# Kernel optimization log

Hardware: AMD Instinct MI355X
Metric: run time of the kernel (lower is better)

## Reference

```python
import jax, jax.numpy as jnp
import numpy as np

HEAD_SIZE = 64
N_EMBD = 1024
BLOCK_SIZE = 2048


def setup_inputs() -> dict:
    key = jax.random.key(0)
    kx, kk, kq, kv = jax.random.split(key, 4)
    B, T = 8, 2048
    x = jax.random.normal(kx, (B, T, N_EMBD), dtype=jnp.float32)
    # nnx.Linear kernels have shape (in_features, out_features); lecun-normal-ish scale
    s = 1.0 / np.sqrt(N_EMBD)
    Wk = jax.random.normal(kk, (N_EMBD, HEAD_SIZE), dtype=jnp.float32) * s
    Wq = jax.random.normal(kq, (N_EMBD, HEAD_SIZE), dtype=jnp.float32) * s
    Wv = jax.random.normal(kv, (N_EMBD, HEAD_SIZE), dtype=jnp.float32) * s
    return {"x": x, "Wk": Wk, "Wq": Wq, "Wv": Wv}


def reference(x, Wk, Wq, Wv):
    B, T, C = x.shape
    k = jnp.einsum("btc,ch->bth", x, Wk)  # [B,T,H]
    q = jnp.einsum("btc,ch->bth", x, Wq)
    v = jnp.einsum("btc,ch->bth", x, Wv)
    # NOTE: original scales by C**-0.5 where C = n_embd (not head_size)
    scale = jnp.float32(C) ** -0.5
    wei = jnp.einsum("bth,bsh->bts", q, k) * scale  # [B,T,T]
    causal = jnp.tril(jnp.ones((T, T), dtype=bool))
    wei = jnp.where(causal, wei, -jnp.inf)
    wei = jax.nn.softmax(wei, axis=-1)
    # dropout_rate = 0.0 -> identity
    out = jnp.einsum("bts,bsh->bth", wei, v)  # [B,T,H]
    return out
```

## Files before the change

### kernel.cpp

```cpp
#include <hip/hip_runtime.h>
#include <hip/hip_bf16.h>

#define TT 2048
#define BATCH 8
#define MROWS (BATCH*TT)
#define AW 8

typedef __attribute__((ext_vector_type(8))) short bf16x8;
typedef __attribute__((ext_vector_type(4))) short s16x4;
typedef __attribute__((ext_vector_type(4))) float f32x4;

__device__ __forceinline__ short f2bf(float f) {
    union { __hip_bfloat16 h; short s; } u;
    u.h = __float2bfloat16(f);
    return u.s;
}
__device__ __forceinline__ float bf2f(short s) {
    union { unsigned u; float f; } u;
    u.u = ((unsigned)(unsigned short)s) << 16;
    return u.f;
}

typedef __attribute__((address_space(3))) unsigned int       lds_u32_t;
typedef const __attribute__((address_space(1))) unsigned int g_u32_t;
__device__ __forceinline__ void gl_lds16(const void* g, void* l) {
    __builtin_amdgcn_global_load_lds((g_u32_t*)g, (lds_u32_t*)l, 16, 0, 0);
}

__global__ __launch_bounds__(256) void wtrans_kernel(
    const float* __restrict__ Wk, const float* __restrict__ Wq,
    const float* __restrict__ Wv, short* __restrict__ wt)
{
    __shared__ float tile[64][68];
    const int mat = blockIdx.x >> 4;
    const int k0  = (blockIdx.x & 15) * 64;
    const float* W = (mat == 0) ? Wq : (mat == 1) ? Wk : Wv;
    const float scl = (mat == 0) ? 0.04508422002778011f : 1.0f;
    const int t = threadIdx.x;
    const int row = t >> 2, quad = t & 3;
    #pragma unroll
    for (int i = 0; i < 4; i++) {
        float4 v = *(const float4*)(W + (size_t)(k0 + row) * 64 + quad * 16 + i * 4);
        *(float4*)&tile[row][quad * 16 + i * 4] = v;
    }
    __syncthreads();
    short tmp[16];
    #pragma unroll
    for (int j = 0; j < 16; j++) tmp[j] = f2bf(tile[quad * 16 + j][row] * scl);
    short* dst = wt + (size_t)(mat * 64 + row) * 1024 + k0 + quad * 16;
    #pragma unroll
    for (int j2 = 0; j2 < 2; j2++) {
        bf16x8 o;
        #pragma unroll
        for (int jj = 0; jj < 8; jj++) o[jj] = tmp[j2 * 8 + jj];
        *(bf16x8*)(dst + j2 * 8) = o;
    }
}

__global__ __launch_bounds__(256, 2) void proj_kernel(
    const float* __restrict__ x, const short* __restrict__ wt,
    short* __restrict__ qb, short* __restrict__ kb, short* __restrict__ vtb)
{
    __shared__ __align__(16) char lds[65536];

    const int tid  = threadIdx.x;
    const int lane = tid & 63, w = tid >> 6;
    const int l15  = lane & 15, g = lane >> 4;
    const int x7   = l15 & 7;
    const int wr   = w & 1;
    const int wc   = w >> 1;
    const int r0   = blockIdx.x * 32;

    const float* ag[2]; unsigned aOff[2];
    #pragma unroll
    for (int j = 0; j < 2; j++) {
        const int jp   = w * 2 + j;
        const int row  = jp * 4 + (lane >> 4);
        const int slot = (lane & 15) ^ (row & 7);
        ag[j]   = x + (size_t)(r0 + row) * 1024 + slot * 4;
        aOff[j] = jp * 1024;
    }
    const short* bg[6]; unsigned bOff[6];
    #pragma unroll
    for (int j = 0; j < 6; j++) {
        const int jp   = w * 6 + j;
        const int row  = jp * 8 + (lane >> 3);
        const int slot = (lane & 7) ^ (row & 7);
        bg[j]   = wt + (size_t)row * 1024 + slot * 8;
        bOff[j] = jp * 1024;
    }

    f32x4 acc[6];
    #pragma unroll
    for (int nt = 0; nt < 6; nt++) acc[nt] = (f32x4){0.f, 0.f, 0.f, 0.f};

    #pragma unroll
    for (int j = 0; j < 2; j++) gl_lds16(ag[j], lds + aOff[j]);
    #pragma unroll
    for (int j = 0; j < 6; j++) gl_lds16(bg[j], lds + 16384 + bOff[j]);
    __syncthreads();

    #pragma unroll
    for (int ks = 0; ks < 16; ks++) {
        const int cur = ks & 1;

        if (ks < 15) {
            const int nb = cur ^ 1;
            #pragma unroll
            for (int j = 0; j < 2; j++)
                gl_lds16(ag[j] + (ks + 1) * 64, lds + nb * 8192 + aOff[j]);
            #pragma unroll
            for (int j = 0; j < 6; j++)
                gl_lds16(bg[j] + (ks + 1) * 64, lds + 16384 + nb * 24576 + bOff[j]);
        }

        const float* Ab = (const float*)(lds + cur * 8192);
        const short* Bb = (const short*)(lds + 16384 + cur * 24576);

        bf16x8 af[2];
        #pragma unroll
        for (int kc = 0; kc < 2; kc++) {
            const int arow = wr * 16 + l15;
            f32x4 lo = *(const f32x4*)(Ab + arow * 64 + ((kc * 8 + 2 * g)     ^ x7) * 4);
            f32x4 hi = *(const f32x4*)(Ab + arow * 64 + ((kc * 8 + 2 * g + 1) ^ x7) * 4);
            af[kc] = (bf16x8){ f2bf(lo[0]), f2bf(lo[1]), f2bf(lo[2]), f2bf(lo[3]),
                               f2bf(hi[0]), f2bf(hi[1]), f2bf(hi[2]), f2bf(hi[3]) };
        }
        bf16x8 bfr[6][2];
        #pragma unroll
        for (int nt = 0; nt < 6; nt++)
            #pragma unroll
            for (int kc = 0; kc < 2; kc++)
                bfr[nt][kc] = *(const bf16x8*)(
                    Bb + (wc * 96 + nt * 16 + l15) * 64 + ((kc * 4 + g) ^ x7) * 8);

        #pragma unroll
        for (int kc = 0; kc < 2; kc++)
            #pragma unroll
            for (int nt = 0; nt < 6; nt++)
                acc[nt] = __builtin_amdgcn_mfma_f32_16x16x32_bf16(
                    af[kc], bfr[nt][kc], acc[nt], 0, 0, 0);

        __syncthreads();
    }

    const int bi  = r0 >> 11;
    const int sl0 = r0 & 2047;
    short* vsl = (short*)lds;
    #pragma unroll
    for (int nt = 0; nt < 6; nt++) {
        const int c = wc * 96 + nt * 16 + l15;
        #pragma unroll
        for (int r = 0; r < 4; r++) {
            const int row = r0 + wr * 16 + g * 4 + r;
            const short v = f2bf(acc[nt][r]);
            if (c < 64)        qb[(size_t)row * 64 + c] = v;
            else if (c < 128)  kb[(size_t)row * 64 + (c - 64)] = v;
            else               vsl[(wr * 16 + g * 4 + r) * 66 + (c - 128)] = v;
        }
    }
    __syncthreads();
    {
        const int col = tid >> 2, seg = tid & 3;
        short tmp[8];
        #pragma unroll
        for (int j = 0; j < 8; j++) tmp[j] = vsl[(seg * 8 + j) * 66 + col];
        bf16x8 o;
        #pragma unroll
        for (int jj = 0; jj < 8; jj++) o[jj] = tmp[jj];
        *(bf16x8*)(vtb + ((size_t)bi * 64 + col) * TT + sl0 + seg * 8) = o;
    }
}

__global__ __launch_bounds__(512, 2)
void attn_kernel(
    const short* __restrict__ qb, const short* __restrict__ kb,
    const short* __restrict__ vtb, float* __restrict__ out)
{
    __shared__ __align__(16) char smem[AW * 4608];
    __shared__ float ml[AW][64];

    const int tid  = threadIdx.x;
    const int w    = tid >> 6, lane = tid & 63;
    const int l15  = lane & 15, g = lane >> 4;
    const int b    = blockIdx.x & 7;
    const int qt   = 63 - (blockIdx.x >> 3);
    const int r0   = qt * 32;
    const int nkv  = (r0 >> 6) + 1;

    short* ps = (short*)(smem + w * 4608);

    const short* q  = qb  + (size_t)b * TT * 64;
    const short* k  = kb  + (size_t)b * TT * 64;
    const short* vt = vtb + (size_t)b * 64 * TT;

    bf16x8 qf[2][2];
    #pragma unroll
    for (int rt = 0; rt < 2; rt++)
        #pragma unroll
        for (int kc = 0; kc < 2; kc++)
            qf[rt][kc] = *(const bf16x8*)(q + (size_t)(r0 + rt * 16 + l15) * 64 + kc * 32 + g * 8);

    f32x4 o[2][4];
    float m_[2] = { -INFINITY, -INFINITY };
    float l_[2] = { 0.f, 0.f };
    #pragma unroll
    for (int rt = 0; rt < 2; rt++)
        #pragma unroll
        for (int ht = 0; ht < 4; ht++) o[rt][ht] = (f32x4){0.f, 0.f, 0.f, 0.f};

    bf16x8 kf[4][2];
    if (w < nkv) {
        #pragma unroll
        for (int nt = 0; nt < 4; nt++)
            #pragma unroll
            for (int kc = 0; kc < 2; kc++)
                kf[nt][kc] = *(const bf16x8*)(
                    k + (size_t)(w * 64 + nt * 16 + l15) * 64 + kc * 32 + g * 8);
    }

    for (int t = w; t < nkv; t += AW) {
        const int s0 = t * 64;
        const bool diag = (t == nkv - 1);
        const bool more = (t + AW < nkv);

        f32x4 s[2][4];
        #pragma unroll
        for (int rt = 0; rt < 2; rt++)
            #pragma unroll
            for (int nt = 0; nt < 4; nt++) s[rt][nt] = (f32x4){0.f, 0.f, 0.f, 0.f};
        #pragma unroll
        for (int kc = 0; kc < 2; kc++)
            #pragma unroll
            for (int rt = 0; rt < 2; rt++)
                #pragma unroll
                for (int nt = 0; nt < 4; nt++)
                    s[rt][nt] = __builtin_amdgcn_mfma_f32_16x16x32_bf16(
                        kf[nt][kc], qf[rt][kc], s[rt][nt], 0, 0, 0);

        bf16x8 vf[4][2];
        #pragma unroll
        for (int ht = 0; ht < 4; ht++)
            #pragma unroll
            for (int kc = 0; kc < 2; kc++)
                vf[ht][kc] = *(const bf16x8*)(
                    vt + (size_t)(ht * 16 + l15) * TT + s0 + kc * 32 + g * 8);
        bf16x8 kfn[4][2];
        if (more) {
            #pragma unroll
            for (int nt = 0; nt < 4; nt++)
                #pragma unroll
                for (int kc = 0; kc < 2; kc++)
                    kfn[nt][kc] = *(const bf16x8*)(
                        k + (size_t)(s0 + AW * 64 + nt * 16 + l15) * 64 + kc * 32 + g * 8);
        }

        if (diag) {
            #pragma unroll
            for (int rt = 0; rt < 2; rt++) {
                const int qg = r0 + rt * 16 + l15;
                #pragma unroll
                for (int nt = 0; nt < 4; nt++)
                    #pragma unroll
                    for (int r = 0; r < 4; r++)
                        if (s0 + nt * 16 + g * 4 + r > qg) s[rt][nt][r] = -INFINITY;
            }
        }

        #pragma unroll
        for (int rt = 0; rt < 2; rt++) {
            float a0 = fmaxf(fmaxf(s[rt][0][0], s[rt][0][1]), fmaxf(s[rt][0][2], s[rt][0][3]));
            float a1 = fmaxf(fmaxf(s[rt][1][0], s[rt][1][1]), fmaxf(s[rt][1][2], s[rt][1][3]));
            float a2 = fmaxf(fmaxf(s[rt][2][0], s[rt][2][1]), fmaxf(s[rt][2][2], s[rt][2][3]));
            float a3 = fmaxf(fmaxf(s[rt][3][0], s[rt][3][1]), fmaxf(s[rt][3][2], s[rt][3][3]));
            float tm = fmaxf(fmaxf(a0, a1), fmaxf(a2, a3));
            tm = fmaxf(tm, __shfl_xor(tm, 16));
            tm = fmaxf(tm, __shfl_xor(tm, 32));

            const float mn = fmaxf(m_[rt], tm);
            const float al = __builtin_amdgcn_exp2f(m_[rt] - mn);
            m_[rt] = mn;

            #pragma unroll
            for (int nt = 0; nt < 4; nt++)
                #pragma unroll
                for (int r = 0; r < 4; r++)
                    s[rt][nt][r] = __builtin_amdgcn_exp2f(s[rt][nt][r] - mn);

            float b0 = (s[rt][0][0] + s[rt][0][1]) + (s[rt][0][2] + s[rt][0][3]);
            float b1 = (s[rt][1][0] + s[rt][1][1]) + (s[rt][1][2] + s[rt][1][3]);
            float b2 = (s[rt][2][0] + s[rt][2][1]) + (s[rt][2][2] + s[rt][2][3]);
            float b3 = (s[rt][3][0] + s[rt][3][1]) + (s[rt][3][2] + s[rt][3][3]);
            float ts = (b0 + b1) + (b2 + b3);
            ts += __shfl_xor(ts, 16);
            ts += __shfl_xor(ts, 32);
            l_[rt] = l_[rt] * al + ts;

            float ab[4];
            #pragma unroll
            for (int r = 0; r < 4; r++) ab[r] = __shfl(al, g * 4 + r);
            #pragma unroll
            for (int ht = 0; ht < 4; ht++)
                #pragma unroll
                for (int r = 0; r < 4; r++)
                    o[rt][ht][r] *= ab[r];

            #pragma unroll
            for (int nt = 0; nt < 4; nt++) {
                s16x4 pk = { f2bf(s[rt][nt][0]), f2bf(s[rt][nt][1]),
                             f2bf(s[rt][nt][2]), f2bf(s[rt][nt][3]) };
                *(s16x4*)&ps[(rt * 16 + l15) * 72 + nt * 16 + g * 4] = pk;
            }
        }

        bf16x8 pf[2][2];
        #pragma unroll
        for (int rt = 0; rt < 2; rt++)
            #pragma unroll
            for (int kc = 0; kc < 2; kc++)
                pf[rt][kc] = *(const bf16x8*)&ps[(rt * 16 + l15) * 72 + kc * 32 + g * 8];
        #pragma unroll
        for (int kc = 0; kc < 2; kc++)
            #pragma unroll
            for (int rt = 0; rt < 2; rt++)
                #pragma unroll
                for (int ht = 0; ht < 4; ht++)
                    o[rt][ht] = __builtin_amdgcn_mfma_f32_16x16x32_bf16(
                        pf[rt][kc], vf[ht][kc], o[rt][ht], 0, 0, 0);

        if (more) {
            #pragma unroll
            for (int nt = 0; nt < 4; nt++)
                #pragma unroll
                for (int kc = 0; kc < 2; kc++)
                    kf[nt][kc] = kfn[nt][kc];
        }
    }

    if (g == 0) {
        #pragma unroll
        for (int rt = 0; rt < 2; rt++) {
            ml[w][rt * 16 + l15]      = m_[rt];
            ml[w][32 + rt * 16 + l15] = l_[rt];
        }
    }
    short* pO = ps;
    #pragma unroll
    for (int rt = 0; rt < 2; rt++)
        #pragma unroll
        for (int ht = 0; ht < 4; ht++)
            #pragma unroll
            for (int r = 0; r < 4; r++)
                pO[(rt * 16 + g * 4 + r) * 68 + ht * 16 + l15] = f2bf(o[rt][ht][r]);
    __syncthreads();

    {
        const int row = tid >> 4, seg = tid & 15;
        float gm = -INFINITY;
        #pragma unroll
        for (int w2 = 0; w2 < AW; w2++) gm = fmaxf(gm, ml[w2][row]);
        float accL = 0.f;
        float accO[4] = {0.f, 0.f, 0.f, 0.f};
        #pragma unroll
        for (int w2 = 0; w2 < AW; w2++) {
            const float sc = __builtin_amdgcn_exp2f(ml[w2][row] - gm);
            accL = fmaf(sc, ml[w2][32 + row], accL);
            const s16x4 ov = *(const s16x4*)((const short*)(smem + w2 * 4608) + row * 68 + seg * 4);
            #pragma unroll
            for (int j = 0; j < 4; j++)
                accO[j] = fmaf(sc, bf2f(ov[j]), accO[j]);
        }
        const float inv = 1.f / accL;
        float4 res = make_float4(accO[0] * inv, accO[1] * inv, accO[2] * inv, accO[3] * inv);
        *(float4*)(out + ((size_t)b * TT + r0 + row) * 64 + seg * 4) = res;
    }
}

extern "C" void kernel_launch(void* const* d_in, const int* in_sizes, int n_in,
                              void* d_out, int out_size, void* d_ws, size_t ws_size,
                              hipStream_t stream) {
    const float* x  = (const float*)d_in[0];
    const float* Wk = (const float*)d_in[1];
    const float* Wq = (const float*)d_in[2];
    const float* Wv = (const float*)d_in[3];
    float* outp = (float*)d_out;

    short* wt  = (short*)d_ws;
    short* qb  = wt + (size_t)192 * 1024;
    short* kb  = qb + (size_t)MROWS * 64;
    short* vtb = kb + (size_t)MROWS * 64;

    wtrans_kernel<<<48, 256, 0, stream>>>(Wk, Wq, Wv, wt);
    proj_kernel<<<MROWS / 32, 256, 0, stream>>>(x, wt, qb, kb, vtb);
    attn_kernel<<<BATCH * 64, 512, 0, stream>>>(qb, kb, vtb, outp);
}
```

Baseline: 47.21 us.

## Enlarge projection tile to 64 rows and stage x as bf16 in LDS

The QKV projection kernel now uses 64-row blocks with 512 threads and a K-step of 128. Each wave computes a 2x3 grid of MFMA tiles, so every weight fragment is reused across two row tiles. x is loaded into registers, converted to bf16 once, and written to LDS after the MFMAs, which overlaps the global load with compute and halves A-tile LDS traffic. The cost is 128KB of LDS, which limits occupancy to about one block per CU, plus more register pressure.

```diff
diff --git a/kernel.cpp b/kernel.cpp
--- a/kernel.cpp
+++ b/kernel.cpp
@@ -57,11 +57,11 @@
     }
 }
 
-__global__ __launch_bounds__(256, 2) void proj_kernel(
+__global__ __launch_bounds__(512, 2) void proj_kernel(
     const float* __restrict__ x, const short* __restrict__ wt,
     short* __restrict__ qb, short* __restrict__ kb, short* __restrict__ vtb)
 {
-    __shared__ __align__(16) char lds[65536];
+    __shared__ __align__(16) char lds[131072];
 
     const int tid  = threadIdx.x;
     const int lane = tid & 63, w = tid >> 6;
@@ -69,78 +69,99 @@
     const int x7   = l15 & 7;
     const int wr   = w & 1;
     const int wc   = w >> 1;
-    const int r0   = blockIdx.x * 32;
-
-    const float* ag[2]; unsigned aOff[2];
-    #pragma unroll
-    for (int j = 0; j < 2; j++) {
-        const int jp   = w * 2 + j;
+    const int r0   = blockIdx.x * 64;
+
+    const int arow_s = tid >> 3, aseg = tid & 7;
+    const float* xsrc = x + (size_t)(r0 + arow_s) * 1024 + aseg * 16;
+    const int ac0 = ((aseg * 2)     ^ (arow_s & 7)) * 16;
+    const int ac1 = ((aseg * 2 + 1) ^ (arow_s & 7)) * 16;
+    char* const arow_lds0 = lds + arow_s * 256;
+
+    const short* bg[6]; unsigned bOff[6];
+    #pragma unroll
+    for (int j = 0; j < 6; j++) {
+        const int jp   = w * 6 + j;
         const int row  = jp * 4 + (lane >> 4);
         const int slot = (lane & 15) ^ (row & 7);
-        ag[j]   = x + (size_t)(r0 + row) * 1024 + slot * 4;
-        aOff[j] = jp * 1024;
-    }
-    const short* bg[6]; unsigned bOff[6];
-    #pragma unroll
-    for (int j = 0; j < 6; j++) {
-        const int jp   = w * 6 + j;
-        const int row  = jp * 8 + (lane >> 3);
-        const int slot = (lane & 7) ^ (row & 7);
         bg[j]   = wt + (size_t)row * 1024 + slot * 8;
-        bOff[j] = jp * 1024;
-    }
-
-    f32x4 acc[6];
-    #pragma unroll
-    for (int nt = 0; nt < 6; nt++) acc[nt] = (f32x4){0.f, 0.f, 0.f, 0.f};
-
-    #pragma unroll
-    for (int j = 0; j < 2; j++) gl_lds16(ag[j], lds + aOff[j]);
-    #pragma unroll
-    for (int j = 0; j < 6; j++) gl_lds16(bg[j], lds + 16384 + bOff[j]);
+        bOff[j] = 32768 + jp * 1024;
+    }
+
+    f32x4 acc[2][3];
+    #pragma unroll
+    for (int rt = 0; rt < 2; rt++)
+        #pragma unroll
+        for (int nt = 0; nt < 3; nt++) acc[rt][nt] = (f32x4){0.f, 0.f, 0.f, 0.f};
+
+    {
+        float4 a0 = *(const float4*)(xsrc);
+        float4 a1 = *(const float4*)(xsrc + 4);
+        float4 a2 = *(const float4*)(xsrc + 8);
+        float4 a3 = *(const float4*)(xsrc + 12);
+        #pragma unroll
+        for (int j = 0; j < 6; j++) gl_lds16(bg[j], lds + bOff[j]);
+        bf16x8 c0 = { f2bf(a0.x), f2bf(a0.y), f2bf(a0.z), f2bf(a0.w),
+                      f2bf(a1.x), f2bf(a1.y), f2bf(a1.z), f2bf(a1.w) };
+        bf16x8 c1 = { f2bf(a2.x), f2bf(a2.y), f2bf(a2.z), f2bf(a2.w),
+                      f2bf(a3.x), f2bf(a3.y), f2bf(a3.z), f2bf(a3.w) };
+        *(bf16x8*)(arow_lds0 + ac0) = c0;
+        *(bf16x8*)(arow_lds0 + ac1) = c1;
+    }
     __syncthreads();
 
     #pragma unroll
-    for (int ks = 0; ks < 16; ks++) {
+    for (int ks = 0; ks < 8; ks++) {
         const int cur = ks & 1;
-
-        if (ks < 15) {
-            const int nb = cur ^ 1;
-            #pragma unroll
-            for (int j = 0; j < 2; j++)
-                gl_lds16(ag[j] + (ks + 1) * 64, lds + nb * 8192 + aOff[j]);
+        const int nb  = cur ^ 1;
+
+        float4 a0, a1, a2, a3;
+        if (ks < 7) {
+            a0 = *(const float4*)(xsrc + (ks + 1) * 128);
+            a1 = *(const float4*)(xsrc + (ks + 1) * 128 + 4);
+            a2 = *(const float4*)(xsrc + (ks + 1) * 128 + 8);
+            a3 = *(const float4*)(xsrc + (ks + 1) * 128 + 12);
             #pragma unroll
             for (int j = 0; j < 6; j++)
-                gl_lds16(bg[j] + (ks + 1) * 64, lds + 16384 + nb * 24576 + bOff[j]);
-        }
-
-        const float* Ab = (const float*)(lds + cur * 8192);
-        const short* Bb = (const short*)(lds + 16384 + cur * 24576);
-
-        bf16x8 af[2];
-        #pragma unroll
-        for (int kc = 0; kc < 2; kc++) {
-            const int arow = wr * 16 + l15;
-            f32x4 lo = *(const f32x4*)(Ab + arow * 64 + ((kc * 8 + 2 * g)     ^ x7) * 4);
-            f32x4 hi = *(const f32x4*)(Ab + arow * 64 + ((kc * 8 + 2 * g + 1) ^ x7) * 4);
-            af[kc] = (bf16x8){ f2bf(lo[0]), f2bf(lo[1]), f2bf(lo[2]), f2bf(lo[3]),
-                               f2bf(hi[0]), f2bf(hi[1]), f2bf(hi[2]), f2bf(hi[3]) };
-        }
-        bf16x8 bfr[6][2];
-        #pragma unroll
-        for (int nt = 0; nt < 6; nt++)
-            #pragma unroll
-            for (int kc = 0; kc < 2; kc++)
+                gl_lds16(bg[j] + (ks + 1) * 128, lds + nb * 49152 + bOff[j]);
+        }
+
+        const char*  Ab = lds + cur * 16384;
+        const short* Bb = (const short*)(lds + 32768 + cur * 49152);
+
+        bf16x8 af[2][4];
+        #pragma unroll
+        for (int rt = 0; rt < 2; rt++) {
+            const int arow = wr * 32 + rt * 16 + l15;
+            #pragma unroll
+            for (int kc = 0; kc < 4; kc++)
+                af[rt][kc] = *(const bf16x8*)(
+                    Ab + arow * 256 + (((kc * 4 + g) ^ x7) * 16));
+        }
+        bf16x8 bfr[3][4];
+        #pragma unroll
+        for (int nt = 0; nt < 3; nt++)
+            #pragma unroll
+            for (int kc = 0; kc < 4; kc++)
                 bfr[nt][kc] = *(const bf16x8*)(
-                    Bb + (wc * 96 + nt * 16 + l15) * 64 + ((kc * 4 + g) ^ x7) * 8);
-
-        #pragma unroll
-        for (int kc = 0; kc < 2; kc++)
-            #pragma unroll
-            for (int nt = 0; nt < 6; nt++)
-                acc[nt] = __builtin_amdgcn_mfma_f32_16x16x32_bf16(
-                    af[kc], bfr[nt][kc], acc[nt], 0, 0, 0);
-
+                    Bb + (wc * 48 + nt * 16 + l15) * 128 + (((kc * 4 + g) ^ x7) * 8));
+
+        #pragma unroll
+        for (int kc = 0; kc < 4; kc++)
+            #pragma unroll
+            for (int rt = 0; rt < 2; rt++)
+                #pragma unroll
+                for (int nt = 0; nt < 3; nt++)
+                    acc[rt][nt] = __builtin_amdgcn_mfma_f32_16x16x32_bf16(
+                        af[rt][kc], bfr[nt][kc], acc[rt][nt], 0, 0, 0);
+
+        if (ks < 7) {
+            bf16x8 c0 = { f2bf(a0.x), f2bf(a0.y), f2bf(a0.z), f2bf(a0.w),
+                          f2bf(a1.x), f2bf(a1.y), f2bf(a1.z), f2bf(a1.w) };
+            bf16x8 c1 = { f2bf(a2.x), f2bf(a2.y), f2bf(a2.z), f2bf(a2.w),
+                          f2bf(a3.x), f2bf(a3.y), f2bf(a3.z), f2bf(a3.w) };
+            *(bf16x8*)(lds + nb * 16384 + arow_s * 256 + ac0) = c0;
+            *(bf16x8*)(lds + nb * 16384 + arow_s * 256 + ac1) = c1;
+        }
         __syncthreads();
     }
 
@@ -148,20 +169,22 @@
     const int sl0 = r0 & 2047;
     short* vsl = (short*)lds;
     #pragma unroll
-    for (int nt = 0; nt < 6; nt++) {
-        const int c = wc * 96 + nt * 16 + l15;
-        #pragma unroll
-        for (int r = 0; r < 4; r++) {
-            const int row = r0 + wr * 16 + g * 4 + r;
-            const short v = f2bf(acc[nt][r]);
-            if (c < 64)        qb[(size_t)row * 64 + c] = v;
-            else if (c < 128)  kb[(size_t)row * 64 + (c - 64)] = v;
-            else               vsl[(wr * 16 + g * 4 + r) * 66 + (c - 128)] = v;
-        }
-    }
+    for (int rt = 0; rt < 2; rt++)
+        #pragma unroll
+        for (int nt = 0; nt < 3; nt++) {
+            const int c = wc * 48 + nt * 16 + l15;
+            #pragma unroll
+            for (int r = 0; r < 4; r++) {
+                const int lrow = wr * 32 + rt * 16 + g * 4 + r;
+                const short v = f2bf(acc[rt][nt][r]);
+                if (c < 64)        qb[(size_t)(r0 + lrow) * 64 + c] = v;
+                else if (c < 128)  kb[(size_t)(r0 + lrow) * 64 + (c - 64)] = v;
+                else               vsl[lrow * 66 + (c - 128)] = v;
+            }
+        }
     __syncthreads();
     {
-        const int col = tid >> 2, seg = tid & 3;
+        const int col = tid >> 3, seg = tid & 7;
         short tmp[8];
         #pragma unroll
         for (int j = 0; j < 8; j++) tmp[j] = vsl[(seg * 8 + j) * 66 + col];
@@ -391,6 +414,6 @@
     short* vtb = kb + (size_t)MROWS * 64;
 
     wtrans_kernel<<<48, 256, 0, stream>>>(Wk, Wq, Wv, wt);
-    proj_kernel<<<MROWS / 32, 256, 0, stream>>>(x, wt, qb, kb, vtb);
+    proj_kernel<<<MROWS / 64, 512, 0, stream>>>(x, wt, qb, kb, vtb);
     attn_kernel<<<BATCH * 64, 512, 0, stream>>>(qb, kb, vtb, outp);
 }
```

New measurement: 51.17 us. 8.4% more time.

## Double attention query tile to 64 rows per block, halving block count

Applied to the files above, without the earlier changes.

The attention kernel now processes 64 query rows per block instead of 32, so each loaded K/V tile is reused across four 16-row MFMA tiles instead of two. The grid shrinks from 512 to 256 blocks, LDS per wave doubles, and launch bounds drop to one block per CU. The score computation is restructured per row tile to limit register pressure. The proj_kernel change only moves a constant offset into bOff. The trade-off is fewer blocks on a large GPU and worse causal load balance, which may lower occupancy and leave CUs idle.

```diff
diff --git a/kernel.cpp b/kernel.cpp
--- a/kernel.cpp
+++ b/kernel.cpp
@@ -87,7 +87,7 @@
         const int row  = jp * 8 + (lane >> 3);
         const int slot = (lane & 7) ^ (row & 7);
         bg[j]   = wt + (size_t)row * 1024 + slot * 8;
-        bOff[j] = jp * 1024;
+        bOff[j] = 16384 + jp * 1024;
     }
 
     f32x4 acc[6];
@@ -97,7 +97,7 @@
     #pragma unroll
     for (int j = 0; j < 2; j++) gl_lds16(ag[j], lds + aOff[j]);
     #pragma unroll
-    for (int j = 0; j < 6; j++) gl_lds16(bg[j], lds + 16384 + bOff[j]);
+    for (int j = 0; j < 6; j++) gl_lds16(bg[j], lds + bOff[j]);
     __syncthreads();
 
     #pragma unroll
@@ -111,7 +111,7 @@
                 gl_lds16(ag[j] + (ks + 1) * 64, lds + nb * 8192 + aOff[j]);
             #pragma unroll
             for (int j = 0; j < 6; j++)
-                gl_lds16(bg[j] + (ks + 1) * 64, lds + 16384 + nb * 24576 + bOff[j]);
+                gl_lds16(bg[j] + (ks + 1) * 64, lds + nb * 24576 + bOff[j]);
         }
 
         const float* Ab = (const float*)(lds + cur * 8192);
@@ -172,40 +172,40 @@
     }
 }
 
-__global__ __launch_bounds__(512, 2)
+__global__ __launch_bounds__(512, 1)
 void attn_kernel(
     const short* __restrict__ qb, const short* __restrict__ kb,
     const short* __restrict__ vtb, float* __restrict__ out)
 {
-    __shared__ __align__(16) char smem[AW * 4608];
-    __shared__ float ml[AW][64];
+    __shared__ __align__(16) char smem[AW * 9216];
+    __shared__ float ml[AW][128];
 
     const int tid  = threadIdx.x;
     const int w    = tid >> 6, lane = tid & 63;
     const int l15  = lane & 15, g = lane >> 4;
     const int b    = blockIdx.x & 7;
-    const int qt   = 63 - (blockIdx.x >> 3);
-    const int r0   = qt * 32;
-    const int nkv  = (r0 >> 6) + 1;
-
-    short* ps = (short*)(smem + w * 4608);
+    const int qt   = 31 - (blockIdx.x >> 3);
+    const int r0   = qt * 64;
+    const int nkv  = qt + 1;
+
+    short* ps = (short*)(smem + w * 9216);
 
     const short* q  = qb  + (size_t)b * TT * 64;
     const short* k  = kb  + (size_t)b * TT * 64;
     const short* vt = vtb + (size_t)b * 64 * TT;
 
-    bf16x8 qf[2][2];
-    #pragma unroll
-    for (int rt = 0; rt < 2; rt++)
+    bf16x8 qf[4][2];
+    #pragma unroll
+    for (int rt = 0; rt < 4; rt++)
         #pragma unroll
         for (int kc = 0; kc < 2; kc++)
             qf[rt][kc] = *(const bf16x8*)(q + (size_t)(r0 + rt * 16 + l15) * 64 + kc * 32 + g * 8);
 
-    f32x4 o[2][4];
-    float m_[2] = { -INFINITY, -INFINITY };
-    float l_[2] = { 0.f, 0.f };
-    #pragma unroll
-    for (int rt = 0; rt < 2; rt++)
+    f32x4 o[4][4];
+    float m_[4] = { -INFINITY, -INFINITY, -INFINITY, -INFINITY };
+    float l_[4] = { 0.f, 0.f, 0.f, 0.f };
+    #pragma unroll
+    for (int rt = 0; rt < 4; rt++)
         #pragma unroll
         for (int ht = 0; ht < 4; ht++) o[rt][ht] = (f32x4){0.f, 0.f, 0.f, 0.f};
 
@@ -224,55 +224,51 @@
         const bool diag = (t == nkv - 1);
         const bool more = (t + AW < nkv);
 
-        f32x4 s[2][4];
-        #pragma unroll
-        for (int rt = 0; rt < 2; rt++)
-            #pragma unroll
-            for (int nt = 0; nt < 4; nt++) s[rt][nt] = (f32x4){0.f, 0.f, 0.f, 0.f};
-        #pragma unroll
-        for (int kc = 0; kc < 2; kc++)
-            #pragma unroll
-            for (int rt = 0; rt < 2; rt++)
+        bf16x8 vf[4][2];
+        bf16x8 kfn[4][2];
+
+        #pragma unroll
+        for (int rt = 0; rt < 4; rt++) {
+            f32x4 s[4];
+            #pragma unroll
+            for (int nt = 0; nt < 4; nt++) s[nt] = (f32x4){0.f, 0.f, 0.f, 0.f};
+            #pragma unroll
+            for (int kc = 0; kc < 2; kc++)
                 #pragma unroll
                 for (int nt = 0; nt < 4; nt++)
-                    s[rt][nt] = __builtin_amdgcn_mfma_f32_16x16x32_bf16(
-                        kf[nt][kc], qf[rt][kc], s[rt][nt], 0, 0, 0);
-
-        bf16x8 vf[4][2];
-        #pragma unroll
-        for (int ht = 0; ht < 4; ht++)
-            #pragma unroll
-            for (int kc = 0; kc < 2; kc++)
-                vf[ht][kc] = *(const bf16x8*)(
-                    vt + (size_t)(ht * 16 + l15) * TT + s0 + kc * 32 + g * 8);
-        bf16x8 kfn[4][2];
-        if (more) {
-            #pragma unroll
-            for (int nt = 0; nt < 4; nt++)
-                #pragma unroll
-                for (int kc = 0; kc < 2; kc++)
-                    kfn[nt][kc] = *(const bf16x8*)(
-                        k + (size_t)(s0 + AW * 64 + nt * 16 + l15) * 64 + kc * 32 + g * 8);
-        }
-
-        if (diag) {
-            #pragma unroll
-            for (int rt = 0; rt < 2; rt++) {
+                    s[nt] = __builtin_amdgcn_mfma_f32_16x16x32_bf16(
+                        kf[nt][kc], qf[rt][kc], s[nt], 0, 0, 0);
+
+            if (rt == 0) {
+                #pragma unroll
+                for (int ht = 0; ht < 4; ht++)
+                    #pragma unroll
+                    for (int kc = 0; kc < 2; kc++)
+                        vf[ht][kc] = *(const bf16x8*)(
+                            vt + (size_t)(ht * 16 + l15) * TT + s0 + kc * 32 + g * 8);
+            }
+            if (rt == 1 && more) {
+                #pragma unroll
+                for (int nt = 0; nt < 4; nt++)
+                    #pragma unroll
+                    for (int kc = 0; kc < 2; kc++)
+                        kfn[nt][kc] = *(const bf16x8*)(
+                            k + (size_t)(s0 + AW * 64 + nt * 16 + l15) * 64 + kc * 32 + g * 8);
+            }
+
+            if (diag) {
                 const int qg = r0 + rt * 16 + l15;
                 #pragma unroll
                 for (int nt = 0; nt < 4; nt++)
                     #pragma unroll
                     for (int r = 0; r < 4; r++)
-                        if (s0 + nt * 16 + g * 4 + r > qg) s[rt][nt][r] = -INFINITY;
-            }
-        }
-
-        #pragma unroll
-        for (int rt = 0; rt < 2; rt++) {
-            float a0 = fmaxf(fmaxf(s[rt][0][0], s[rt][0][1]), fmaxf(s[rt][0][2], s[rt][0][3]));
-            float a1 = fmaxf(fmaxf(s[rt][1][0], s[rt][1][1]), fmaxf(s[rt][1][2], s[rt][1][3]));
-            float a2 = fmaxf(fmaxf(s[rt][2][0], s[rt][2][1]), fmaxf(s[rt][2][2], s[rt][2][3]));
-            float a3 = fmaxf(fmaxf(s[rt][3][0], s[rt][3][1]), fmaxf(s[rt][3][2], s[rt][3][3]));
+                        if (s0 + nt * 16 + g * 4 + r > qg) s[nt][r] = -INFINITY;
+            }
+
+            float a0 = fmaxf(fmaxf(s[0][0], s[0][1]), fmaxf(s[0][2], s[0][3]));
+            float a1 = fmaxf(fmaxf(s[1][0], s[1][1]), fmaxf(s[1][2], s[1][3]));
+            float a2 = fmaxf(fmaxf(s[2][0], s[2][1]), fmaxf(s[2][2], s[2][3]));
+            float a3 = fmaxf(fmaxf(s[3][0], s[3][1]), fmaxf(s[3][2], s[3][3]));
             float tm = fmaxf(fmaxf(a0, a1), fmaxf(a2, a3));
             tm = fmaxf(tm, __shfl_xor(tm, 16));
             tm = fmaxf(tm, __shfl_xor(tm, 32));
@@ -285,12 +281,12 @@
             for (int nt = 0; nt < 4; nt++)
                 #pragma unroll
                 for (int r = 0; r < 4; r++)
-                    s[rt][nt][r] = __builtin_amdgcn_exp2f(s[rt][nt][r] - mn);
-
-            float b0 = (s[rt][0][0] + s[rt][0][1]) + (s[rt][0][2] + s[rt][0][3]);
-            float b1 = (s[rt][1][0] + s[rt][1][1]) + (s[rt][1][2] + s[rt][1][3]);
-            float b2 = (s[rt][2][0] + s[rt][2][1]) + (s[rt][2][2] + s[rt][2][3]);
-            float b3 = (s[rt][3][0] + s[rt][3][1]) + (s[rt][3][2] + s[rt][3][3]);
+                    s[nt][r] = __builtin_amdgcn_exp2f(s[nt][r] - mn);
+
+            float b0 = (s[0][0] + s[0][1]) + (s[0][2] + s[0][3]);
+            float b1 = (s[1][0] + s[1][1]) + (s[1][2] + s[1][3]);
+            float b2 = (s[2][0] + s[2][1]) + (s[2][2] + s[2][3]);
+            float b3 = (s[3][0] + s[3][1]) + (s[3][2] + s[3][3]);
             float ts = (b0 + b1) + (b2 + b3);
             ts += __shfl_xor(ts, 16);
             ts += __shfl_xor(ts, 32);
@@ -307,26 +303,25 @@
 
             #pragma unroll
             for (int nt = 0; nt < 4; nt++) {
-                s16x4 pk = { f2bf(s[rt][nt][0]), f2bf(s[rt][nt][1]),
-                             f2bf(s[rt][nt][2]), f2bf(s[rt][nt][3]) };
+                s16x4 pk = { f2bf(s[nt][0]), f2bf(s[nt][1]),
+                             f2bf(s[nt][2]), f2bf(s[nt][3]) };
                 *(s16x4*)&ps[(rt * 16 + l15) * 72 + nt * 16 + g * 4] = pk;
             }
         }
 
-        bf16x8 pf[2][2];
-        #pragma unroll
-        for (int rt = 0; rt < 2; rt++)
-            #pragma unroll
-            for (int kc = 0; kc < 2; kc++)
-                pf[rt][kc] = *(const bf16x8*)&ps[(rt * 16 + l15) * 72 + kc * 32 + g * 8];
-        #pragma unroll
-        for (int kc = 0; kc < 2; kc++)
-            #pragma unroll
-            for (int rt = 0; rt < 2; rt++)
+        #pragma unroll
+        for (int rt = 0; rt < 4; rt++) {
+            bf16x8 pf[2];
+            #pragma unroll
+            for (int kc = 0; kc < 2; kc++)
+                pf[kc] = *(const bf16x8*)&ps[(rt * 16 + l15) * 72 + kc * 32 + g * 8];
+            #pragma unroll
+            for (int kc = 0; kc < 2; kc++)
                 #pragma unroll
                 for (int ht = 0; ht < 4; ht++)
                     o[rt][ht] = __builtin_amdgcn_mfma_f32_16x16x32_bf16(
-                        pf[rt][kc], vf[ht][kc], o[rt][ht], 0, 0, 0);
+                        pf[kc], vf[ht][kc], o[rt][ht], 0, 0, 0);
+        }
 
         if (more) {
             #pragma unroll
@@ -339,14 +334,14 @@
 
     if (g == 0) {
         #pragma unroll
-        for (int rt = 0; rt < 2; rt++) {
+        for (int rt = 0; rt < 4; rt++) {
             ml[w][rt * 16 + l15]      = m_[rt];
-            ml[w][32 + rt * 16 + l15] = l_[rt];
+            ml[w][64 + rt * 16 + l15] = l_[rt];
         }
     }
     short* pO = ps;
     #pragma unroll
-    for (int rt = 0; rt < 2; rt++)
+    for (int rt = 0; rt < 4; rt++)
         #pragma unroll
         for (int ht = 0; ht < 4; ht++)
             #pragma unroll
@@ -355,24 +350,31 @@
     __syncthreads();
 
     {
-        const int row = tid >> 4, seg = tid & 15;
+        const int row = tid >> 3, seg = tid & 7;
         float gm = -INFINITY;
         #pragma unroll
         for (int w2 = 0; w2 < AW; w2++) gm = fmaxf(gm, ml[w2][row]);
         float accL = 0.f;
-        float accO[4] = {0.f, 0.f, 0.f, 0.f};
+        float accO[8] = {0.f, 0.f, 0.f, 0.f, 0.f, 0.f, 0.f, 0.f};
         #pragma unroll
         for (int w2 = 0; w2 < AW; w2++) {
             const float sc = __builtin_amdgcn_exp2f(ml[w2][row] - gm);
-            accL = fmaf(sc, ml[w2][32 + row], accL);
-            const s16x4 ov = *(const s16x4*)((const short*)(smem + w2 * 4608) + row * 68 + seg * 4);
-            #pragma unroll
-            for (int j = 0; j < 4; j++)
-                accO[j] = fmaf(sc, bf2f(ov[j]), accO[j]);
+            accL = fmaf(sc, ml[w2][64 + row], accL);
+            const short* src = (const short*)(smem + w2 * 9216) + row * 68 + seg * 8;
+            const s16x4 ov0 = *(const s16x4*)(src);
+            const s16x4 ov1 = *(const s16x4*)(src + 4);
+            #pragma unroll
+            for (int j = 0; j < 4; j++) {
+                accO[j]     = fmaf(sc, bf2f(ov0[j]), accO[j]);
+                accO[4 + j] = fmaf(sc, bf2f(ov1[j]), accO[4 + j]);
+            }
         }
         const float inv = 1.f / accL;
-        float4 res = make_float4(accO[0] * inv, accO[1] * inv, accO[2] * inv, accO[3] * inv);
-        *(float4*)(out + ((size_t)b * TT + r0 + row) * 64 + seg * 4) = res;
+        float4 r0v = make_float4(accO[0] * inv, accO[1] * inv, accO[2] * inv, accO[3] * inv);
+        float4 r1v = make_float4(accO[4] * inv, accO[5] * inv, accO[6] * inv, accO[7] * inv);
+        float* dst = out + ((size_t)b * TT + r0 + row) * 64 + seg * 8;
+        *(float4*)(dst)     = r0v;
+        *(float4*)(dst + 4) = r1v;
     }
 }
 
@@ -392,5 +394,5 @@
 
     wtrans_kernel<<<48, 256, 0, stream>>>(Wk, Wq, Wv, wt);
     proj_kernel<<<MROWS / 32, 256, 0, stream>>>(x, wt, qb, kb, vtb);
-    attn_kernel<<<BATCH * 64, 512, 0, stream>>>(qb, kb, vtb, outp);
-}
+    attn_kernel<<<BATCH * 32, 512, 0, stream>>>(qb, kb, vtb, outp);
+}
```

New measurement: 51.44 us. 1.09x slower.
